# Kernel tuning notes

Measured on AMD Instinct MI355X. Metric: run time of the kernel, lower is better.

## Reference

```python
import jax, jax.numpy as jnp
import numpy as np

B, P, H, N, D, K = 1024, 1024, 4096, 32, 512, 128


def setup_inputs() -> dict:
    key = jax.random.key(0)
    k1, k2, k3, k4, k5 = jax.random.split(key, 5)
    return {
        "proximal_input": jax.random.normal(k1, (B, P), dtype=jnp.float32),
        "distal_input": jax.random.normal(k2, (B, D), dtype=jnp.float32),
        "W": jax.random.normal(k3, (H, P), dtype=jnp.float32) / np.sqrt(P),
        "b": jax.random.normal(k4, (H,), dtype=jnp.float32) / np.sqrt(P),
        "distal": jax.random.normal(k5, (H, N, D), dtype=jnp.float32),
        "k": K,
    }


def reference(proximal_input, distal_input, W, b, distal, k):
    # proximal path: standard linear -> (B, H)
    proximal_output = proximal_input @ W.T + b
    # per-hidden-unit dendrite projections -> (H, B, N)
    distal_output = jnp.einsum('bd,hnd->hbn', distal_input, distal)
    # pick dominant dendrite by absolute value, keep its signed value
    abs_max_idx = jnp.argmax(jnp.abs(distal_output), axis=-1)          # (H, B)
    distal_max = jnp.take_along_axis(
        distal_output, abs_max_idx[..., None], axis=-1)[..., 0].T      # (B, H)
    # sigmoid gate modulates proximal activations
    result = proximal_output * jax.nn.sigmoid(distal_max)              # (B, H)
    # keep only top-k per row (scatter-built 0/1 mask, as in the original)
    _, top_idxs = jax.lax.top_k(result, k)                             # (B, k)
    rows = jnp.arange(result.shape[0])[:, None]
    mask = jnp.zeros_like(result).at[rows, top_idxs].set(1.0)
    return result * mask
```

## Files before the change

### kernel.cpp

```cpp
#include <hip/hip_runtime.h>
#include <cstdint>
#include <cmath>

#define Bsz  1024
#define Pdim 1024
#define Hdim 4096
#define Ndim 32
#define Ddim 512
#define Ktop 128

typedef _Float16 f16x8 __attribute__((ext_vector_type(8)));
typedef float    f32x4 __attribute__((ext_vector_type(4)));

#define GLDS(gsrc, ldst)                                                        \
  __builtin_amdgcn_global_load_lds(                                             \
      (const __attribute__((address_space(1))) unsigned int*)(gsrc),            \
      (__attribute__((address_space(3))) unsigned int*)(ldst), 16, 0, 0)

#define WS_NEEDED 270532608ull

__global__ __launch_bounds__(256) void proximal_gemm(
    const float* __restrict__ pin, const float* __restrict__ W,
    const float* __restrict__ bias, float* __restrict__ out)
{
  __shared__ float Blds[32 * 256];
  __shared__ float Alds[32 * 32];
  const int t  = threadIdx.x;
  const int l  = t & 63;
  const int wv = t >> 6;

  const int ell   = blockIdx.x;
  const int xcd   = ell & 7;
  const int q     = ell >> 3;
  const int htile = xcd * 2 + (q >> 5);
  const int btile = q & 31;
  const int h0 = htile * 256, b0 = btile * 32;

  float acc[8][4];
#pragma unroll
  for (int i = 0; i < 8; i++)
    for (int j = 0; j < 4; j++) acc[i][j] = 0.f;

  const float* wrow = W + (size_t)(h0 + t) * Pdim;
  const int ab = t >> 3, ak = (t & 7) * 4;
  const float* arow = pin + (size_t)(b0 + ab) * Pdim + ak;

  for (int kt = 0; kt < Pdim / 32; ++kt) {
    const int p0 = kt * 32;
    float wbuf[32];
#pragma unroll
    for (int f = 0; f < 8; f++) {
      float4 v = *(const float4*)(wrow + p0 + f * 4);
      wbuf[f * 4 + 0] = v.x; wbuf[f * 4 + 1] = v.y;
      wbuf[f * 4 + 2] = v.z; wbuf[f * 4 + 3] = v.w;
    }
    float4 av = *(const float4*)(arow + p0);
    __syncthreads();
#pragma unroll
    for (int f = 0; f < 32; f++) Blds[f * 256 + t] = wbuf[f];
    Alds[(ak + 0) * 32 + ab] = av.x;
    Alds[(ak + 1) * 32 + ab] = av.y;
    Alds[(ak + 2) * 32 + ab] = av.z;
    Alds[(ak + 3) * 32 + ab] = av.w;
    __syncthreads();
#pragma unroll
    for (int k = 0; k < 32; k++) {
      float4 bv  = *(const float4*)&Blds[k * 256 + 4 * l];
      float4 alo = *(const float4*)&Alds[k * 32 + 8 * wv];
      float4 ahi = *(const float4*)&Alds[k * 32 + 8 * wv + 4];
      float a0[8] = {alo.x, alo.y, alo.z, alo.w, ahi.x, ahi.y, ahi.z, ahi.w};
#pragma unroll
      for (int i = 0; i < 8; i++) {
        acc[i][0] += a0[i] * bv.x;
        acc[i][1] += a0[i] * bv.y;
        acc[i][2] += a0[i] * bv.z;
        acc[i][3] += a0[i] * bv.w;
      }
    }
  }
  float4 bb = *(const float4*)(bias + h0 + 4 * l);
#pragma unroll
  for (int i = 0; i < 8; i++) {
    float4 o;
    o.x = acc[i][0] + bb.x;
    o.y = acc[i][1] + bb.y;
    o.z = acc[i][2] + bb.z;
    o.w = acc[i][3] + bb.w;
    *(float4*)(out + (size_t)(b0 + 8 * wv + i) * Hdim + h0 + 4 * l) = o;
  }
}

__global__ __launch_bounds__(256) void convert_distal(
    const float* __restrict__ src, char* __restrict__ dstA)
{
  const int gid = blockIdx.x * 256 + threadIdx.x;
  const int np_ = gid >> 6;
  const int e   = (gid & 63) * 8;
  float4 v0 = *(const float4*)(src + (size_t)np_ * Ddim + e);
  float4 v1 = *(const float4*)(src + (size_t)np_ * Ddim + e + 4);
  const int ntile = np_ >> 7, r = np_ & 127, ks = e >> 5, k = e & 31;
  char* base = dstA + (size_t)(ntile * 16 + ks) * 16384;
  const int off = (r >> 4) * 1024 + (((k >> 3) * 16 + (r & 15)) * 16);
  const float f[8] = {v0.x, v0.y, v0.z, v0.w, v1.x, v1.y, v1.z, v1.w};
  f16x8 hi, lo;
#pragma unroll
  for (int j = 0; j < 8; j++) {
    const _Float16 h = (_Float16)f[j];
    hi[j] = h;
    lo[j] = (_Float16)((f[j] - (float)h) * 256.f);
  }
  *(f16x8*)(base + off)        = hi;
  *(f16x8*)(base + 8192 + off) = lo;
}

__global__ __launch_bounds__(256) void convert_din(
    const float* __restrict__ src, char* __restrict__ dstB)
{
  const int gid = blockIdx.x * 256 + threadIdx.x;
  const int b   = gid >> 6;
  const int e   = (gid & 63) * 8;
  float4 v0 = *(const float4*)(src + (size_t)b * Ddim + e);
  float4 v1 = *(const float4*)(src + (size_t)b * Ddim + e + 4);
  const int btile = b >> 7, c = b & 127, ks = e >> 5, k = e & 31;
  char* base = dstB + (size_t)(btile * 16 + ks) * 16384;
  const int off = (c >> 4) * 1024 + (((k >> 3) * 16 + (c & 15)) * 16);
  const float f[8] = {v0.x, v0.y, v0.z, v0.w, v1.x, v1.y, v1.z, v1.w};
  f16x8 hi, lo;
#pragma unroll
  for (int j = 0; j < 8; j++) {
    const _Float16 h = (_Float16)f[j];
    hi[j] = h;
    lo[j] = (_Float16)((f[j] - (float)h) * 256.f);
  }
  *(f16x8*)(base + off)        = hi;
  *(f16x8*)(base + 8192 + off) = lo;
}

__global__ __launch_bounds__(256, 2) void distal_mfma(
    const char* __restrict__ Aw, const char* __restrict__ Bw,
    float* __restrict__ out)
{
  __shared__ __align__(16) char lds[2][32768];
  const int t = threadIdx.x, lane = t & 63, wv = t >> 6;
  const int g = lane >> 4, c15 = lane & 15;
  const int wrow0 = (wv >> 1) * 64, wcol0 = (wv & 1) * 64;

  const int blk = blockIdx.x;
  const int xcd = blk & 7, q = blk >> 3;
  const int ntile = xcd * 128 + (q >> 3);
  const int btile = q & 7;

  f32x4 acc[4][4], accx[4][4];
#pragma unroll
  for (int mi = 0; mi < 4; mi++)
#pragma unroll
    for (int ni = 0; ni < 4; ni++) {
      acc[mi][ni]  = (f32x4){0.f, 0.f, 0.f, 0.f};
      accx[mi][ni] = (f32x4){0.f, 0.f, 0.f, 0.f};
    }

  const char* Abase = Aw + (size_t)(ntile * 16) * 16384;
  const char* Bbase = Bw + (size_t)(btile * 16) * 16384;

  auto STAGE = [&](char* bufp, int ks) {
    const char* As = Abase + ks * 16384;
    const char* Bs = Bbase + ks * 16384;
#pragma unroll
    for (int j = 0; j < 4; j++) {
      const int ch = j * 4 + wv;
      GLDS(As + ch * 1024 + lane * 16, bufp + ch * 1024);
      GLDS(Bs + ch * 1024 + lane * 16, bufp + 16384 + ch * 1024);
    }
  };

  STAGE(lds[0], 0);
  __syncthreads();

  int cur = 0;
  for (int ks = 0; ks < 16; ++ks) {
    if (ks < 15) STAGE(lds[cur ^ 1], ks + 1);

    const char* L = lds[cur];
    f16x8 ah[4], al[4], bh[4], bl[4];
#pragma unroll
    for (int mi = 0; mi < 4; mi++) {
      const int f = (wv >> 1) * 4 + mi;
      ah[mi] = *(const f16x8*)(L + f * 1024 + lane * 16);
      al[mi] = *(const f16x8*)(L + 8192 + f * 1024 + lane * 16);
    }
#pragma unroll
    for (int ni = 0; ni < 4; ni++) {
      const int f = (wv & 1) * 4 + ni;
      bh[ni] = *(const f16x8*)(L + 16384 + f * 1024 + lane * 16);
      bl[ni] = *(const f16x8*)(L + 24576 + f * 1024 + lane * 16);
    }
#pragma unroll
    for (int mi = 0; mi < 4; mi++)
#pragma unroll
      for (int ni = 0; ni < 4; ni++) {
        acc[mi][ni]  = __builtin_amdgcn_mfma_f32_16x16x32_f16(ah[mi], bh[ni], acc[mi][ni],  0, 0, 0);
        accx[mi][ni] = __builtin_amdgcn_mfma_f32_16x16x32_f16(ah[mi], bl[ni], accx[mi][ni], 0, 0, 0);
        accx[mi][ni] = __builtin_amdgcn_mfma_f32_16x16x32_f16(al[mi], bh[ni], accx[mi][ni], 0, 0, 0);
      }

    __syncthreads();
    cur ^= 1;
  }

#pragma unroll
  for (int hh = 0; hh < 2; ++hh) {
#pragma unroll
    for (int ni = 0; ni < 4; ++ni) {
      float bestA = -1.f, bestV = 0.f;
      int   bestN = 999;
#pragma unroll
      for (int m2 = 0; m2 < 2; ++m2) {
        const int mi = hh * 2 + m2;
#pragma unroll
        for (int reg = 0; reg < 4; ++reg) {
          const float v = acc[mi][ni][reg] + accx[mi][ni][reg] * 0.00390625f;
          const float a = fabsf(v);
          const int   n = m2 * 16 + g * 4 + reg;
          if (a > bestA) { bestA = a; bestV = v; bestN = n; }
        }
      }
#pragma unroll
      for (int m = 16; m <= 32; m <<= 1) {
        const float oa = __shfl_xor(bestA, m, 64);
        const float ov = __shfl_xor(bestV, m, 64);
        const int   on = __shfl_xor(bestN, m, 64);
        if (oa > bestA || (oa == bestA && on < bestN)) {
          bestA = oa; bestV = ov; bestN = on;
        }
      }
      if (g == 0) {
        const int bcol = btile * 128 + wcol0 + ni * 16 + c15;
        const int h    = ntile * 4 + (wv >> 1) * 2 + hh;
        const float gate = 1.f / (1.f + expf(-bestV));
        out[(size_t)bcol * Hdim + h] *= gate;
      }
    }
  }
}

__global__ __launch_bounds__(256) void distal_gate_fb(
    const float* __restrict__ din, const float* __restrict__ distal,
    float* __restrict__ out)
{
  __shared__ float Blds[32 * 256];
  __shared__ float Alds[32 * 32];
  const int t  = threadIdx.x;
  const int l  = t & 63;
  const int wv = t >> 6;
  const int ell   = blockIdx.x;
  const int xcd   = ell & 7;
  const int q     = ell >> 3;
  const int htile = xcd * 64 + (q >> 5);
  const int btile = q & 31;
  const int n0 = htile * 256, b0 = btile * 32;

  float acc[8][4];
#pragma unroll
  for (int i = 0; i < 8; i++)
    for (int j = 0; j < 4; j++) acc[i][j] = 0.f;

  const float* brow = distal + (size_t)(n0 + t) * Ddim;
  const int ab = t >> 3, ak = (t & 7) * 4;
  const float* arow = din + (size_t)(b0 + ab) * Ddim + ak;

  for (int kt = 0; kt < Ddim / 32; ++kt) {
    const int d0 = kt * 32;
    float wbuf[32];
#pragma unroll
    for (int f = 0; f < 8; f++) {
      float4 v = *(const float4*)(brow + d0 + f * 4);
      wbuf[f * 4 + 0] = v.x; wbuf[f * 4 + 1] = v.y;
      wbuf[f * 4 + 2] = v.z; wbuf[f * 4 + 3] = v.w;
    }
    float4 av = *(const float4*)(arow + d0);
    __syncthreads();
#pragma unroll
    for (int f = 0; f < 32; f++) Blds[f * 256 + t] = wbuf[f];
    Alds[(ak + 0) * 32 + ab] = av.x;
    Alds[(ak + 1) * 32 + ab] = av.y;
    Alds[(ak + 2) * 32 + ab] = av.z;
    Alds[(ak + 3) * 32 + ab] = av.w;
    __syncthreads();
#pragma unroll
    for (int k = 0; k < 32; k++) {
      float4 bv  = *(const float4*)&Blds[k * 256 + 4 * l];
      float4 alo = *(const float4*)&Alds[k * 32 + 8 * wv];
      float4 ahi = *(const float4*)&Alds[k * 32 + 8 * wv + 4];
      float a0[8] = {alo.x, alo.y, alo.z, alo.w, ahi.x, ahi.y, ahi.z, ahi.w};
#pragma unroll
      for (int i = 0; i < 8; i++) {
        acc[i][0] += a0[i] * bv.x;
        acc[i][1] += a0[i] * bv.y;
        acc[i][2] += a0[i] * bv.z;
        acc[i][3] += a0[i] * bv.w;
      }
    }
  }
  const int i0  = l & 7;
  const int grp = l >> 3;
  float v = 0.f;
#pragma unroll
  for (int bi = 0; bi < 8; bi++) {
    float bav = fabsf(acc[bi][0]);
    float bv_ = acc[bi][0];
    int   bn  = 4 * i0;
#pragma unroll
    for (int j = 1; j < 4; j++) {
      float av2 = fabsf(acc[bi][j]);
      if (av2 > bav) { bav = av2; bv_ = acc[bi][j]; bn = 4 * i0 + j; }
    }
#pragma unroll
    for (int m = 1; m < 8; m <<= 1) {
      float oav = __shfl_xor(bav, m, 64);
      float ov  = __shfl_xor(bv_, m, 64);
      int   on  = __shfl_xor(bn,  m, 64);
      if (oav > bav || (oav == bav && on < bn)) { bav = oav; bv_ = ov; bn = on; }
    }
    if (bi == i0) v = bv_;
  }
  const float gate = 1.f / (1.f + expf(-v));
  const size_t idx = (size_t)(b0 + 8 * wv + i0) * Hdim + (size_t)htile * 8 + grp;
  out[idx] *= gate;
}

__device__ __forceinline__ unsigned keyf(float f) {
  unsigned u = __float_as_uint(f);
  return (u & 0x80000000u) ? ~u : (u | 0x80000000u);
}

__global__ __launch_bounds__(256) void topk_mask(float* __restrict__ out)
{
  __shared__ float vals[Hdim];
  __shared__ unsigned hist[256];
  __shared__ unsigned sc[4];
  __shared__ unsigned s_prefix, s_kk;
  const int t = threadIdx.x;
  float* row = out + (size_t)blockIdx.x * Hdim;

#pragma unroll
  for (int qq = 0; qq < 4; qq++) {
    float4 v = *(const float4*)(row + qq * 1024 + t * 4);
    *(float4*)&vals[qq * 1024 + t * 4] = v;
  }
  if (t == 0) { s_prefix = 0u; s_kk = Ktop; }
  __syncthreads();

  for (int shift = 24; shift >= 0; shift -= 8) {
    hist[t] = 0u;
    __syncthreads();
    const unsigned prefix = s_prefix;
    const unsigned maskhi = (shift == 24) ? 0u : (0xFFFFFFFFu << (shift + 8));
    for (int c = 0; c < 16; c++) {
      unsigned u = keyf(vals[c * 256 + t]);
      if ((u & maskhi) == prefix)
        atomicAdd(&hist[(u >> shift) & 255u], 1u);
    }
    __syncthreads();
    if (t == 0) {
      unsigned kk = s_kk, cum = 0;
      int bin = 255;
      for (; bin > 0; --bin) {
        unsigned c = hist[bin];
        if (cum + c >= kk) break;
        cum += c;
      }
      s_kk = kk - cum;
      s_prefix = prefix | ((unsigned)bin << shift);
    }
    __syncthreads();
  }
  const unsigned T  = s_prefix;
  const unsigned kk = s_kk;

  const int lane = t & 63, w = t >> 6;
  unsigned running = 0;
  for (int c = 0; c < 16; c++) {
    const int h = c * 256 + t;
    const float v = vals[h];
    const unsigned u = keyf(v);
    const bool tie = (u == T);
    unsigned long long m = __ballot(tie);
    unsigned lpfx = (unsigned)__popcll(m & ((1ull << lane) - 1ull));
    if (lane == 0) sc[w] = (unsigned)__popcll(m);
    __syncthreads();
    unsigned off = 0;
#pragma unroll
    for (int ww = 0; ww < 4; ww++) if (ww < w) off += sc[ww];
    const unsigned rank = running + off + lpfx;
    row[h] = (u > T) ? v : ((tie && rank < kk) ? v : 0.f);
    const unsigned tot = sc[0] + sc[1] + sc[2] + sc[3];
    __syncthreads();
    running += tot;
  }
}

extern "C" void kernel_launch(void* const* d_in, const int* in_sizes, int n_in,
                              void* d_out, int out_size, void* d_ws, size_t ws_size,
                              hipStream_t stream)
{
  (void)in_sizes; (void)n_in; (void)out_size;
  const float* pin  = (const float*)d_in[0];
  const float* dinp = (const float*)d_in[1];
  const float* W    = (const float*)d_in[2];
  const float* bias = (const float*)d_in[3];
  const float* dst  = (const float*)d_in[4];
  float* out = (float*)d_out;

  hipLaunchKernelGGL(proximal_gemm, dim3(512), dim3(256), 0, stream, pin, W, bias, out);

  if (ws_size >= WS_NEEDED) {
    char* Aw = (char*)d_ws;
    char* Bw = (char*)d_ws + 268435456ull;
    hipLaunchKernelGGL(convert_distal, dim3(32768), dim3(256), 0, stream, dst,  Aw);
    hipLaunchKernelGGL(convert_din,    dim3(256),   dim3(256), 0, stream, dinp, Bw);
    hipLaunchKernelGGL(distal_mfma,    dim3(8192),  dim3(256), 0, stream, Aw, Bw, out);
  } else {
    hipLaunchKernelGGL(distal_gate_fb, dim3(16384), dim3(256), 0, stream, dinp, dst, out);
  }

  hipLaunchKernelGGL(topk_mask, dim3(Bsz), dim3(256), 0, stream, out);
}
```

Before: 699.3 us.

## Move proximal GEMM to split-fp16 MFMA and share a generic convert kernel

Replaces the scalar-FP32 proximal GEMM with an MFMA kernel that uses the same hi/lo fp16 split as the distal path. W and the proximal input are first converted into tiled fp16 images in the workspace by a generic convert kernel. The MFMA inner loops are reordered to load B fragments per column and are wrapped in s_setprio raised priority. Adds four conversion passes and reuses workspace regions sequentially. The old scalar GEMM is kept only for the small-workspace fallback.

```diff
diff --git a/kernel.cpp b/kernel.cpp
--- a/kernel.cpp
+++ b/kernel.cpp
@@ -19,6 +19,224 @@
 
 #define WS_NEEDED 270532608ull
 
+__global__ __launch_bounds__(256) void convert_img(
+    const float* __restrict__ src, char* __restrict__ dst, int kcbits)
+{
+  const int gid  = blockIdx.x * 256 + threadIdx.x;
+  const int row  = gid >> kcbits;
+  const int e    = (gid & ((1 << kcbits) - 1)) * 8;
+  const int Krow = 8 << kcbits;
+  float4 v0 = *(const float4*)(src + (size_t)row * Krow + e);
+  float4 v1 = *(const float4*)(src + (size_t)row * Krow + e + 4);
+  const int tile = row >> 7, r = row & 127, ks = e >> 5, k = e & 31;
+  char* base = dst + (size_t)(tile * (Krow >> 5) + ks) * 16384;
+  const int off = (r >> 4) * 1024 + ((k >> 3) * 16 + (r & 15)) * 16;
+  const float f[8] = {v0.x, v0.y, v0.z, v0.w, v1.x, v1.y, v1.z, v1.w};
+  f16x8 hi, lo;
+#pragma unroll
+  for (int j = 0; j < 8; j++) {
+    const _Float16 h = (_Float16)f[j];
+    hi[j] = h;
+    lo[j] = (_Float16)((f[j] - (float)h) * 256.f);
+  }
+  *(f16x8*)(base + off)        = hi;
+  *(f16x8*)(base + 8192 + off) = lo;
+}
+
+__global__ __launch_bounds__(256, 2) void proximal_mfma(
+    const char* __restrict__ Aw, const char* __restrict__ Bw,
+    const float* __restrict__ bias, float* __restrict__ out)
+{
+  __shared__ __align__(16) char lds[2][32768];
+  const int t = threadIdx.x, lane = t & 63, wv = t >> 6;
+  const int g = lane >> 4, c15 = lane & 15;
+  const int wrow0 = (wv >> 1) * 64, wcol0 = (wv & 1) * 64;
+
+  const int blk = blockIdx.x;
+  const int xcd = blk & 7, q = blk >> 3;
+  const int htile = xcd * 4 + (q >> 3);
+  const int btile = q & 7;
+  const int h0 = htile * 128, b0 = btile * 128;
+
+  f32x4 acc[4][4], accx[4][4];
+#pragma unroll
+  for (int mi = 0; mi < 4; mi++)
+#pragma unroll
+    for (int ni = 0; ni < 4; ni++) {
+      acc[mi][ni]  = (f32x4){0.f, 0.f, 0.f, 0.f};
+      accx[mi][ni] = (f32x4){0.f, 0.f, 0.f, 0.f};
+    }
+
+  const char* Abase = Aw + (size_t)(htile * 32) * 16384;
+  const char* Bbase = Bw + (size_t)(btile * 32) * 16384;
+
+  auto STAGE = [&](char* bufp, int ks) {
+    const char* As = Abase + ks * 16384;
+    const char* Bs = Bbase + ks * 16384;
+#pragma unroll
+    for (int j = 0; j < 4; j++) {
+      const int ch = j * 4 + wv;
+      GLDS(As + ch * 1024 + lane * 16, bufp + ch * 1024);
+      GLDS(Bs + ch * 1024 + lane * 16, bufp + 16384 + ch * 1024);
+    }
+  };
+
+  STAGE(lds[0], 0);
+  __syncthreads();
+
+  int cur = 0;
+  for (int ks = 0; ks < 32; ++ks) {
+    if (ks < 31) STAGE(lds[cur ^ 1], ks + 1);
+
+    const char* L = lds[cur];
+    f16x8 ah[4], al[4];
+#pragma unroll
+    for (int mi = 0; mi < 4; mi++) {
+      const int f = (wv >> 1) * 4 + mi;
+      ah[mi] = *(const f16x8*)(L + f * 1024 + lane * 16);
+      al[mi] = *(const f16x8*)(L + 8192 + f * 1024 + lane * 16);
+    }
+    __builtin_amdgcn_s_setprio(1);
+#pragma unroll
+    for (int ni = 0; ni < 4; ni++) {
+      const int f = (wv & 1) * 4 + ni;
+      const f16x8 bh = *(const f16x8*)(L + 16384 + f * 1024 + lane * 16);
+      const f16x8 bl = *(const f16x8*)(L + 24576 + f * 1024 + lane * 16);
+#pragma unroll
+      for (int mi = 0; mi < 4; mi++) {
+        acc[mi][ni]  = __builtin_amdgcn_mfma_f32_16x16x32_f16(ah[mi], bh, acc[mi][ni],  0, 0, 0);
+        accx[mi][ni] = __builtin_amdgcn_mfma_f32_16x16x32_f16(ah[mi], bl, accx[mi][ni], 0, 0, 0);
+        accx[mi][ni] = __builtin_amdgcn_mfma_f32_16x16x32_f16(al[mi], bh, accx[mi][ni], 0, 0, 0);
+      }
+    }
+    __builtin_amdgcn_s_setprio(0);
+    __syncthreads();
+    cur ^= 1;
+  }
+
+#pragma unroll
+  for (int mi = 0; mi < 4; ++mi) {
+    const int hb = h0 + wrow0 + mi * 16 + g * 4;
+    const float4 bb = *(const float4*)(bias + hb);
+#pragma unroll
+    for (int ni = 0; ni < 4; ++ni) {
+      const int bcol = b0 + wcol0 + ni * 16 + c15;
+      float4 o;
+      o.x = acc[mi][ni][0] + accx[mi][ni][0] * 0.00390625f + bb.x;
+      o.y = acc[mi][ni][1] + accx[mi][ni][1] * 0.00390625f + bb.y;
+      o.z = acc[mi][ni][2] + accx[mi][ni][2] * 0.00390625f + bb.z;
+      o.w = acc[mi][ni][3] + accx[mi][ni][3] * 0.00390625f + bb.w;
+      *(float4*)(out + (size_t)bcol * Hdim + hb) = o;
+    }
+  }
+}
+
+__global__ __launch_bounds__(256, 2) void distal_mfma(
+    const char* __restrict__ Aw, const char* __restrict__ Bw,
+    float* __restrict__ out)
+{
+  __shared__ __align__(16) char lds[2][32768];
+  const int t = threadIdx.x, lane = t & 63, wv = t >> 6;
+  const int g = lane >> 4, c15 = lane & 15;
+  const int wrow0 = (wv >> 1) * 64, wcol0 = (wv & 1) * 64;
+
+  const int blk = blockIdx.x;
+  const int xcd = blk & 7, q = blk >> 3;
+  const int ntile = xcd * 128 + (q >> 3);
+  const int btile = q & 7;
+
+  f32x4 acc[4][4], accx[4][4];
+#pragma unroll
+  for (int mi = 0; mi < 4; mi++)
+#pragma unroll
+    for (int ni = 0; ni < 4; ni++) {
+      acc[mi][ni]  = (f32x4){0.f, 0.f, 0.f, 0.f};
+      accx[mi][ni] = (f32x4){0.f, 0.f, 0.f, 0.f};
+    }
+
+  const char* Abase = Aw + (size_t)(ntile * 16) * 16384;
+  const char* Bbase = Bw + (size_t)(btile * 16) * 16384;
+
+  auto STAGE = [&](char* bufp, int ks) {
+    const char* As = Abase + ks * 16384;
+    const char* Bs = Bbase + ks * 16384;
+#pragma unroll
+    for (int j = 0; j < 4; j++) {
+      const int ch = j * 4 + wv;
+      GLDS(As + ch * 1024 + lane * 16, bufp + ch * 1024);
+      GLDS(Bs + ch * 1024 + lane * 16, bufp + 16384 + ch * 1024);
+    }
+  };
+
+  STAGE(lds[0], 0);
+  __syncthreads();
+
+  int cur = 0;
+  for (int ks = 0; ks < 16; ++ks) {
+    if (ks < 15) STAGE(lds[cur ^ 1], ks + 1);
+
+    const char* L = lds[cur];
+    f16x8 ah[4], al[4];
+#pragma unroll
+    for (int mi = 0; mi < 4; mi++) {
+      const int f = (wv >> 1) * 4 + mi;
+      ah[mi] = *(const f16x8*)(L + f * 1024 + lane * 16);
+      al[mi] = *(const f16x8*)(L + 8192 + f * 1024 + lane * 16);
+    }
+    __builtin_amdgcn_s_setprio(1);
+#pragma unroll
+    for (int ni = 0; ni < 4; ni++) {
+      const int f = (wv & 1) * 4 + ni;
+      const f16x8 bh = *(const f16x8*)(L + 16384 + f * 1024 + lane * 16);
+      const f16x8 bl = *(const f16x8*)(L + 24576 + f * 1024 + lane * 16);
+#pragma unroll
+      for (int mi = 0; mi < 4; mi++) {
+        acc[mi][ni]  = __builtin_amdgcn_mfma_f32_16x16x32_f16(ah[mi], bh, acc[mi][ni],  0, 0, 0);
+        accx[mi][ni] = __builtin_amdgcn_mfma_f32_16x16x32_f16(ah[mi], bl, accx[mi][ni], 0, 0, 0);
+        accx[mi][ni] = __builtin_amdgcn_mfma_f32_16x16x32_f16(al[mi], bh, accx[mi][ni], 0, 0, 0);
+      }
+    }
+    __builtin_amdgcn_s_setprio(0);
+    __syncthreads();
+    cur ^= 1;
+  }
+
+#pragma unroll
+  for (int hh = 0; hh < 2; ++hh) {
+#pragma unroll
+    for (int ni = 0; ni < 4; ++ni) {
+      float bestA = -1.f, bestV = 0.f;
+      int   bestN = 999;
+#pragma unroll
+      for (int m2 = 0; m2 < 2; ++m2) {
+        const int mi = hh * 2 + m2;
+#pragma unroll
+        for (int reg = 0; reg < 4; ++reg) {
+          const float v = acc[mi][ni][reg] + accx[mi][ni][reg] * 0.00390625f;
+          const float a = fabsf(v);
+          const int   n = m2 * 16 + g * 4 + reg;
+          if (a > bestA) { bestA = a; bestV = v; bestN = n; }
+        }
+      }
+#pragma unroll
+      for (int m = 16; m <= 32; m <<= 1) {
+        const float oa = __shfl_xor(bestA, m, 64);
+        const float ov = __shfl_xor(bestV, m, 64);
+        const int   on = __shfl_xor(bestN, m, 64);
+        if (oa > bestA || (oa == bestA && on < bestN)) {
+          bestA = oa; bestV = ov; bestN = on;
+        }
+      }
+      if (g == 0) {
+        const int bcol = btile * 128 + wcol0 + ni * 16 + c15;
+        const int h    = ntile * 4 + (wv >> 1) * 2 + hh;
+        const float gate = 1.f / (1.f + expf(-bestV));
+        out[(size_t)bcol * Hdim + h] *= gate;
+      }
+    }
+  }
+}
+
 __global__ __launch_bounds__(256) void proximal_gemm(
     const float* __restrict__ pin, const float* __restrict__ W,
     const float* __restrict__ bias, float* __restrict__ out)
@@ -28,7 +246,6 @@
   const int t  = threadIdx.x;
   const int l  = t & 63;
   const int wv = t >> 6;
-
   const int ell   = blockIdx.x;
   const int xcd   = ell & 7;
   const int q     = ell >> 3;
@@ -87,159 +304,6 @@
     o.z = acc[i][2] + bb.z;
     o.w = acc[i][3] + bb.w;
     *(float4*)(out + (size_t)(b0 + 8 * wv + i) * Hdim + h0 + 4 * l) = o;
-  }
-}
-
-__global__ __launch_bounds__(256) void convert_distal(
-    const float* __restrict__ src, char* __restrict__ dstA)
-{
-  const int gid = blockIdx.x * 256 + threadIdx.x;
-  const int np_ = gid >> 6;
-  const int e   = (gid & 63) * 8;
-  float4 v0 = *(const float4*)(src + (size_t)np_ * Ddim + e);
-  float4 v1 = *(const float4*)(src + (size_t)np_ * Ddim + e + 4);
-  const int ntile = np_ >> 7, r = np_ & 127, ks = e >> 5, k = e & 31;
-  char* base = dstA + (size_t)(ntile * 16 + ks) * 16384;
-  const int off = (r >> 4) * 1024 + (((k >> 3) * 16 + (r & 15)) * 16);
-  const float f[8] = {v0.x, v0.y, v0.z, v0.w, v1.x, v1.y, v1.z, v1.w};
-  f16x8 hi, lo;
-#pragma unroll
-  for (int j = 0; j < 8; j++) {
-    const _Float16 h = (_Float16)f[j];
-    hi[j] = h;
-    lo[j] = (_Float16)((f[j] - (float)h) * 256.f);
-  }
-  *(f16x8*)(base + off)        = hi;
-  *(f16x8*)(base + 8192 + off) = lo;
-}
-
-__global__ __launch_bounds__(256) void convert_din(
-    const float* __restrict__ src, char* __restrict__ dstB)
-{
-  const int gid = blockIdx.x * 256 + threadIdx.x;
-  const int b   = gid >> 6;
-  const int e   = (gid & 63) * 8;
-  float4 v0 = *(const float4*)(src + (size_t)b * Ddim + e);
-  float4 v1 = *(const float4*)(src + (size_t)b * Ddim + e + 4);
-  const int btile = b >> 7, c = b & 127, ks = e >> 5, k = e & 31;
-  char* base = dstB + (size_t)(btile * 16 + ks) * 16384;
-  const int off = (c >> 4) * 1024 + (((k >> 3) * 16 + (c & 15)) * 16);
-  const float f[8] = {v0.x, v0.y, v0.z, v0.w, v1.x, v1.y, v1.z, v1.w};
-  f16x8 hi, lo;
-#pragma unroll
-  for (int j = 0; j < 8; j++) {
-    const _Float16 h = (_Float16)f[j];
-    hi[j] = h;
-    lo[j] = (_Float16)((f[j] - (float)h) * 256.f);
-  }
-  *(f16x8*)(base + off)        = hi;
-  *(f16x8*)(base + 8192 + off) = lo;
-}
-
-__global__ __launch_bounds__(256, 2) void distal_mfma(
-    const char* __restrict__ Aw, const char* __restrict__ Bw,
-    float* __restrict__ out)
-{
-  __shared__ __align__(16) char lds[2][32768];
-  const int t = threadIdx.x, lane = t & 63, wv = t >> 6;
-  const int g = lane >> 4, c15 = lane & 15;
-  const int wrow0 = (wv >> 1) * 64, wcol0 = (wv & 1) * 64;
-
-  const int blk = blockIdx.x;
-  const int xcd = blk & 7, q = blk >> 3;
-  const int ntile = xcd * 128 + (q >> 3);
-  const int btile = q & 7;
-
-  f32x4 acc[4][4], accx[4][4];
-#pragma unroll
-  for (int mi = 0; mi < 4; mi++)
-#pragma unroll
-    for (int ni = 0; ni < 4; ni++) {
-      acc[mi][ni]  = (f32x4){0.f, 0.f, 0.f, 0.f};
-      accx[mi][ni] = (f32x4){0.f, 0.f, 0.f, 0.f};
-    }
-
-  const char* Abase = Aw + (size_t)(ntile * 16) * 16384;
-  const char* Bbase = Bw + (size_t)(btile * 16) * 16384;
-
-  auto STAGE = [&](char* bufp, int ks) {
-    const char* As = Abase + ks * 16384;
-    const char* Bs = Bbase + ks * 16384;
-#pragma unroll
-    for (int j = 0; j < 4; j++) {
-      const int ch = j * 4 + wv;
-      GLDS(As + ch * 1024 + lane * 16, bufp + ch * 1024);
-      GLDS(Bs + ch * 1024 + lane * 16, bufp + 16384 + ch * 1024);
-    }
-  };
-
-  STAGE(lds[0], 0);
-  __syncthreads();
-
-  int cur = 0;
-  for (int ks = 0; ks < 16; ++ks) {
-    if (ks < 15) STAGE(lds[cur ^ 1], ks + 1);
-
-    const char* L = lds[cur];
-    f16x8 ah[4], al[4], bh[4], bl[4];
-#pragma unroll
-    for (int mi = 0; mi < 4; mi++) {
-      const int f = (wv >> 1) * 4 + mi;
-      ah[mi] = *(const f16x8*)(L + f * 1024 + lane * 16);
-      al[mi] = *(const f16x8*)(L + 8192 + f * 1024 + lane * 16);
-    }
-#pragma unroll
-    for (int ni = 0; ni < 4; ni++) {
-      const int f = (wv & 1) * 4 + ni;
-      bh[ni] = *(const f16x8*)(L + 16384 + f * 1024 + lane * 16);
-      bl[ni] = *(const f16x8*)(L + 24576 + f * 1024 + lane * 16);
-    }
-#pragma unroll
-    for (int mi = 0; mi < 4; mi++)
-#pragma unroll
-      for (int ni = 0; ni < 4; ni++) {
-        acc[mi][ni]  = __builtin_amdgcn_mfma_f32_16x16x32_f16(ah[mi], bh[ni], acc[mi][ni],  0, 0, 0);
-        accx[mi][ni] = __builtin_amdgcn_mfma_f32_16x16x32_f16(ah[mi], bl[ni], accx[mi][ni], 0, 0, 0);
-        accx[mi][ni] = __builtin_amdgcn_mfma_f32_16x16x32_f16(al[mi], bh[ni], accx[mi][ni], 0, 0, 0);
-      }
-
-    __syncthreads();
-    cur ^= 1;
-  }
-
-#pragma unroll
-  for (int hh = 0; hh < 2; ++hh) {
-#pragma unroll
-    for (int ni = 0; ni < 4; ++ni) {
-      float bestA = -1.f, bestV = 0.f;
-      int   bestN = 999;
-#pragma unroll
-      for (int m2 = 0; m2 < 2; ++m2) {
-        const int mi = hh * 2 + m2;
-#pragma unroll
-        for (int reg = 0; reg < 4; ++reg) {
-          const float v = acc[mi][ni][reg] + accx[mi][ni][reg] * 0.00390625f;
-          const float a = fabsf(v);
-          const int   n = m2 * 16 + g * 4 + reg;
-          if (a > bestA) { bestA = a; bestV = v; bestN = n; }
-        }
-      }
-#pragma unroll
-      for (int m = 16; m <= 32; m <<= 1) {
-        const float oa = __shfl_xor(bestA, m, 64);
-        const float ov = __shfl_xor(bestV, m, 64);
-        const int   on = __shfl_xor(bestN, m, 64);
-        if (oa > bestA || (oa == bestA && on < bestN)) {
-          bestA = oa; bestV = ov; bestN = on;
-        }
-      }
-      if (g == 0) {
-        const int bcol = btile * 128 + wcol0 + ni * 16 + c15;
-        const int h    = ntile * 4 + (wv >> 1) * 2 + hh;
-        const float gate = 1.f / (1.f + expf(-bestV));
-        out[(size_t)bcol * Hdim + h] *= gate;
-      }
-    }
   }
 }
 
@@ -411,15 +475,16 @@
   const float* dst  = (const float*)d_in[4];
   float* out = (float*)d_out;
 
-  hipLaunchKernelGGL(proximal_gemm, dim3(512), dim3(256), 0, stream, pin, W, bias, out);
-
   if (ws_size >= WS_NEEDED) {
-    char* Aw = (char*)d_ws;
-    char* Bw = (char*)d_ws + 268435456ull;
-    hipLaunchKernelGGL(convert_distal, dim3(32768), dim3(256), 0, stream, dst,  Aw);
-    hipLaunchKernelGGL(convert_din,    dim3(256),   dim3(256), 0, stream, dinp, Bw);
-    hipLaunchKernelGGL(distal_mfma,    dim3(8192),  dim3(256), 0, stream, Aw, Bw, out);
+    char* ws = (char*)d_ws;
+    hipLaunchKernelGGL(convert_img,   dim3(2048),  dim3(256), 0, stream, W,   ws,             7);
+    hipLaunchKernelGGL(convert_img,   dim3(512),   dim3(256), 0, stream, pin, ws + 16777216,  7);
+    hipLaunchKernelGGL(proximal_mfma, dim3(256),   dim3(256), 0, stream, ws, ws + 16777216, bias, out);
+    hipLaunchKernelGGL(convert_img,   dim3(32768), dim3(256), 0, stream, dst,  ws,             6);
+    hipLaunchKernelGGL(convert_img,   dim3(256),   dim3(256), 0, stream, dinp, ws + 268435456, 6);
+    hipLaunchKernelGGL(distal_mfma,   dim3(8192),  dim3(256), 0, stream, ws, ws + 268435456, out);
   } else {
+    hipLaunchKernelGGL(proximal_gemm, dim3(512),   dim3(256), 0, stream, pin, W, bias, out);
     hipLaunchKernelGGL(distal_gate_fb, dim3(16384), dim3(256), 0, stream, dinp, dst, out);
   }
 
```

Result: faster. 597.7 us (-14.5%).
